# Performance work log

Hardware: AMD Instinct MI355X
Metric: run time of the kernel (lower is better)

Reference implementation:

```python
import jax, jax.numpy as jnp
import numpy as np

B, L, H, W = 4, 16, 4096, 128   # W == nfeat == nclass (required by out.reshape)
NHID = 256

def setup_inputs() -> dict:
    key = jax.random.key(0)
    k1, k2, k3, k4 = jax.random.split(key, 4)
    x = jax.random.normal(k1, (B, L, H, W), dtype=jnp.float32)
    # row-normalized-ish dense adjacency stand-in for the sparse normalized adj
    adj = jax.random.uniform(k2, (H, H), dtype=jnp.float32) / H
    # GraphConvolution params: support = input @ Wk; out = adj @ support + bk
    W1 = jax.random.normal(k3, (W, NHID), dtype=jnp.float32) / np.sqrt(W)
    b1 = jnp.zeros((NHID,), dtype=jnp.float32)
    W2 = jax.random.normal(k4, (NHID, W), dtype=jnp.float32) / np.sqrt(NHID)
    b2 = jnp.zeros((W,), dtype=jnp.float32)
    return {"x": x, "adj": adj, "W1": W1, "b1": b1, "W2": W2, "b2": b2}

def reference(x, adj, W1, b1, W2, b2):
    Bv, Lv, Hv, Wv = x.shape
    xf = x.reshape(Bv * Lv, Hv, Wv)                      # [BL, H, F]
    # gc1: transform then aggregate, fused over all slices (replaces per-slice loop)
    h = jnp.einsum('nm,bmf->bnf', adj, xf @ W1) + b1     # [BL, H, nhid]
    h = jax.nn.relu(h)
    # dropout: inference mode (training=False) -> identity
    out = jnp.einsum('nm,bmf->bnf', adj, h @ W2) + b2    # [BL, H, nclass]
    out = out.reshape(Bv, Lv, Hv, Wv)
    return jax.nn.log_softmax(out, axis=-1)
```

## Files before the change

kernel.cpp:

```cpp
#include <hip/hip_runtime.h>

typedef __attribute__((ext_vector_type(8))) __bf16 bf16x8;
typedef __attribute__((ext_vector_type(4))) float f32x4;
typedef __attribute__((ext_vector_type(16))) float f32x16;
typedef __attribute__((ext_vector_type(4))) int i32x4;
typedef __attribute__((ext_vector_type(8))) int i32x8;
typedef union { i32x8 v8; i32x4 v4[2]; } opnd;

__device__ __forceinline__ ushort f2b(float f) {
  union { float f; unsigned u; } v; v.f = f;
  unsigned u = v.u + 0x7fffu + ((v.u >> 16) & 1u);
  return (ushort)(u >> 16);
}

__device__ __forceinline__ unsigned fp4q(float v) {
  float a = __builtin_fabsf(v);
  unsigned q = (unsigned)(a > 0.25f) + (a > 0.75f) + (a > 1.25f) + (a > 1.75f)
             + (a > 2.5f) + (a > 3.5f) + (a > 5.0f);
  return q | (v < 0.0f ? 8u : 0u);
}
__device__ __forceinline__ ushort fp4pk4(float v0, float v1, float v2, float v3) {
  return (ushort)(fp4q(v0) | (fp4q(v1) << 4) | (fp4q(v2) << 8) | (fp4q(v3) << 12));
}

__device__ __forceinline__ long tiled_addr(long r, long k, int nkb) {
  return (((r >> 5) * nkb) + (k >> 6)) * 2048 + ((k & 16) ? 1024 : 0)
       + (((r & 31) + (((k >> 5) & 1) << 5)) << 4) + (k & 15);
}
__device__ __forceinline__ long tile4_addr(long r, long k, int nkb) {
  return (((r >> 5) * nkb) + (k >> 6)) * 1024
       + (((r & 31) + (((k >> 5) & 1) << 5)) << 4) + ((k & 31) >> 1);
}

__device__ __forceinline__ long remap_wg(int lin, int nwg, int gx) {
  long g = lin;
  if ((nwg & 7) == 0) {
    int cpx = nwg >> 3;
    int gyx = cpx / gx;
    int xcd = lin & 7, idx = lin >> 3;
    if ((gx & 3) == 0 && gyx >= 4 && (gyx & 3) == 0) {
      int st = idx >> 4, wi = idx & 15;
      int nstr = gx >> 2;
      int str = st % nstr, stc = st / nstr;
      int r = str * 4 + (wi & 3);
      int c2 = stc * 4 + (wi >> 2);
      g = (long)xcd * cpx + (long)c2 * gx + r;
    } else {
      g = (long)xcd * cpx + idx;
    }
  }
  return g;
}

__global__ __launch_bounds__(256) void cvtAdj4t(const float* __restrict__ in,
                                                unsigned char* __restrict__ out, long n) {
  long i = ((long)blockIdx.x * 256 + threadIdx.x) * 8;
  if (i >= n) return;
  float4 a = *(const float4*)(in + i);
  float4 b = *(const float4*)(in + i + 4);
  const float S = 24576.0f;
  ushort p0 = fp4pk4(a.x * S, a.y * S, a.z * S, a.w * S);
  ushort p1 = fp4pk4(b.x * S, b.y * S, b.z * S, b.w * S);
  long r = i >> 12;
  long k = i & 4095;
  *(int*)(out + tile4_addr(r, k, 64)) = (int)p0 | ((int)p1 << 16);
}

__global__ __launch_bounds__(256) void cvtX4t(const float* __restrict__ X,
                                              unsigned char* __restrict__ out4) {
  __shared__ float tile[32][33];
  const int tid = threadIdx.x;
  const long bl = blockIdx.z;
  const int m0 = blockIdx.y * 32;
  const int w0 = blockIdx.x * 32;
  const float* xb = X + (bl * 4096 + m0) * 128 + w0;
  int row = tid >> 3, cg = tid & 7;
  float4 v = *(const float4*)(xb + (long)row * 128 + cg * 4);
  tile[row][cg * 4 + 0] = v.x;
  tile[row][cg * 4 + 1] = v.y;
  tile[row][cg * 4 + 2] = v.z;
  tile[row][cg * 4 + 3] = v.w;
  __syncthreads();
  if (tid < 128) {
    int wv = tid & 31, mg = tid >> 5;
    unsigned word = 0;
#pragma unroll
    for (int i = 0; i < 8; ++i)
      word |= fp4q(tile[mg * 8 + i][wv]) << (4 * i);
    long r = bl * 128 + w0 + wv;
    long k = m0 + mg * 8;
    *(int*)(out4 + tile4_addr(r, k, 64)) = (int)word;
  }
}

__global__ __launch_bounds__(256) void prep_params(const float* __restrict__ W1,
                                                   const float* __restrict__ W2,
                                                   unsigned char* __restrict__ W1T8,
                                                   unsigned char* __restrict__ W2T8) {
  int idx = blockIdx.x * 256 + threadIdx.x;
  if (idx < 32768) {
    int f = idx >> 7, wv = idx & 127;
    float v = W1[wv * 256 + f] * 16.0f;
    int pk = __builtin_amdgcn_cvt_pk_fp8_f32(v, v, 0, 0);
    W1T8[tiled_addr(f, wv, 2)] = (unsigned char)(pk & 0xff);
  } else {
    int t = idx - 32768;
    int cc = t >> 8, f = t & 255;
    float v = W2[f * 128 + cc] * 16.0f;
    int pk = __builtin_amdgcn_cvt_pk_fp8_f32(v, v, 0, 0);
    W2T8[tiled_addr(cc, f, 4)] = (unsigned char)(pk & 0xff);
  }
}

__global__ __launch_bounds__(256, 3) void gemmS1(const unsigned char* __restrict__ A4,
                                                 const unsigned char* __restrict__ X4,
                                                 const unsigned char* __restrict__ W1T8,
                                                 const unsigned char* __restrict__ W2T8,
                                                 unsigned char* __restrict__ t2T4,
                                                 const float* __restrict__ b1,
                                                 int K, int gx) {
  __shared__ unsigned char S1buf[16384];
  __shared__ unsigned char hbuf[32768];
  const int tid = threadIdx.x;
  const int l = tid & 63;
  const int w = tid >> 6;
  long g = remap_wg(blockIdx.x, gridDim.x, gx);
  const long row0 = (g % gx) * 128;
  const long bl = g / gx;
  const int nkb = K >> 6;
  const int wr = w >> 1, wc = w & 1;
  const unsigned char* pA = A4 + (((row0 >> 5) + wr * 2) * (long)nkb) * 1024 + l * 16;
  const unsigned char* pB = X4 + ((bl * 4 + wc * 2) * (long)nkb) * 1024 + l * 16;

  f32x16 acc[2][2] = {};
  opnd aA[2], bA[2], aB[2], bB[2];
  const i32x4 z4 = {0, 0, 0, 0};
#pragma unroll
  for (int fi = 0; fi < 2; ++fi) {
    aA[fi].v4[1] = z4; aB[fi].v4[1] = z4;
    bA[fi].v4[1] = z4; bB[fi].v4[1] = z4;
  }

#define LOADG(KT, AV, BV) do { long off_ = (long)(KT) * 1024;                         \
    _Pragma("unroll") for (int fi = 0; fi < 2; ++fi)                                  \
      AV[fi].v4[0] = *(const i32x4*)(pA + (long)fi * nkb * 1024 + off_);              \
    _Pragma("unroll") for (int j = 0; j < 2; ++j)                                     \
      BV[j].v4[0] = *(const i32x4*)(pB + (long)j * nkb * 1024 + off_);                \
  } while (0)

#define MFMAS(AV, BV) do {                                                            \
    __builtin_amdgcn_s_setprio(1);                                                    \
    _Pragma("unroll") for (int fi = 0; fi < 2; ++fi)                                  \
      _Pragma("unroll") for (int j = 0; j < 2; ++j)                                   \
        acc[fi][j] = __builtin_amdgcn_mfma_scale_f32_32x32x64_f8f6f4(                 \
            AV[fi].v8, BV[j].v8, acc[fi][j], 4, 4, 0, 127, 0, 127);                   \
    __builtin_amdgcn_s_setprio(0); } while (0)

  const int nkt = K >> 6;
  LOADG(0, aA, bA);
  int kt = 0;
  for (; kt < nkt - 2; kt += 2) {
    LOADG(kt + 1, aB, bB);
    MFMAS(aA, bA);
    LOADG(kt + 2, aA, bA);
    MFMAS(aB, bB);
  }
  LOADG(nkt - 1, aB, bB);
  MFMAS(aA, bA);
  MFMAS(aB, bB);
#undef LOADG
#undef MFMAS

  const int hi = l >> 5;
#pragma unroll
  for (int fi = 0; fi < 2; ++fi) {
#pragma unroll
    for (int j = 0; j < 2; ++j) {
      int w_in = wc * 64 + j * 32 + (l & 31);
#pragma unroll
      for (int r = 0; r < 16; ++r) {
        int n = wr * 64 + fi * 32 + (r & 3) + 8 * (r >> 2) + 4 * hi;
        float v = acc[fi][j][r] * 0.125f;
        int pk = __builtin_amdgcn_cvt_pk_fp8_f32(v, v, 0, 0);
        S1buf[tiled_addr(n, w_in, 2)] = (unsigned char)(pk & 0xff);
      }
    }
  }
  __syncthreads();

#pragma unroll
  for (int hh = 0; hh < 2; ++hh) {
#pragma unroll
    for (int fi = 0; fi < 2; ++fi)
#pragma unroll
      for (int jb = 0; jb < 2; ++jb) acc[fi][jb] = (f32x16){};
#pragma unroll
    for (int kt1 = 0; kt1 < 2; ++kt1) {
#pragma unroll
      for (int jb = 0; jb < 2; ++jb) {
        opnd bw;
        const unsigned char* pW = W1T8 + (long)((hh * 4 + wc * 2 + jb) * 2 + kt1) * 2048 + l * 16;
        bw.v4[0] = *(const i32x4*)(pW);
        bw.v4[1] = *(const i32x4*)(pW + 1024);
#pragma unroll
        for (int fi = 0; fi < 2; ++fi) {
          opnd ah;
          const unsigned char* pS = S1buf + (long)((wr * 2 + fi) * 2 + kt1) * 2048 + l * 16;
          ah.v4[0] = *(const i32x4*)(pS);
          ah.v4[1] = *(const i32x4*)(pS + 1024);
          acc[fi][jb] = __builtin_amdgcn_mfma_scale_f32_32x32x64_f8f6f4(
              ah.v8, bw.v8, acc[fi][jb], 0, 0, 0, 127, 0, 127);
        }
      }
    }
#pragma unroll
    for (int fi = 0; fi < 2; ++fi) {
#pragma unroll
      for (int jb = 0; jb < 2; ++jb) {
        int f = hh * 128 + wc * 64 + jb * 32 + (l & 31);
        float bb = b1[f];
#pragma unroll
        for (int r = 0; r < 16; ++r) {
          int n = wr * 64 + fi * 32 + (r & 3) + 8 * (r >> 2) + 4 * hi;
          float v = fmaxf(acc[fi][jb][r] * (1.0f / 49152.0f) + bb, 0.0f) * 128.0f;
          int pk = __builtin_amdgcn_cvt_pk_fp8_f32(v, v, 0, 0);
          hbuf[tiled_addr(n, f, 4)] = (unsigned char)(pk & 0xff);
        }
      }
    }
  }
  __syncthreads();

#pragma unroll
  for (int fi = 0; fi < 2; ++fi)
#pragma unroll
    for (int jb = 0; jb < 2; ++jb) acc[fi][jb] = (f32x16){};
#pragma unroll
  for (int kt2 = 0; kt2 < 4; ++kt2) {
#pragma unroll
    for (int jb = 0; jb < 2; ++jb) {
      opnd bw;
      const unsigned char* pW = W2T8 + (long)((wc * 2 + jb) * 4 + kt2) * 2048 + l * 16;
      bw.v4[0] = *(const i32x4*)(pW);
      bw.v4[1] = *(const i32x4*)(pW + 1024);
#pragma unroll
      for (int fi = 0; fi < 2; ++fi) {
        opnd ah;
        const unsigned char* pH = hbuf + (long)((wr * 2 + fi) * 4 + kt2) * 2048 + l * 16;
        ah.v4[0] = *(const i32x4*)(pH);
        ah.v4[1] = *(const i32x4*)(pH + 1024);
        acc[fi][jb] = __builtin_amdgcn_mfma_scale_f32_32x32x64_f8f6f4(
            ah.v8, bw.v8, acc[fi][jb], 0, 0, 0, 127, 0, 127);
      }
    }
  }
  unsigned char* ob = t2T4 + bl * 262144;
#pragma unroll
  for (int fi = 0; fi < 2; ++fi) {
#pragma unroll
    for (int jb = 0; jb < 2; ++jb) {
      int cc = wc * 64 + jb * 32 + (l & 31);
#pragma unroll
      for (int run = 0; run < 4; ++run) {
        long n0 = row0 + wr * 64 + fi * 32 + 8 * run + 4 * hi;
        const float s = 0.125f;
        ushort pk = fp4pk4(acc[fi][jb][run * 4 + 0] * s, acc[fi][jb][run * 4 + 1] * s,
                           acc[fi][jb][run * 4 + 2] * s, acc[fi][jb][run * 4 + 3] * s);
        *(ushort*)(ob + tile4_addr(cc, n0, 64)) = pk;
      }
    }
  }
}

__global__ __launch_bounds__(512) void gemm256sm(const unsigned char* __restrict__ A4,
                                                 const unsigned char* __restrict__ B4,
                                                 float* __restrict__ out,
                                                 const float* __restrict__ bias,
                                                 float ooScale, int K, int gx,
                                                 int chunkBase) {
  __shared__ unsigned char ring[32768];
  const int tid = threadIdx.x;
  const int l = tid & 63;
  const int w = tid >> 6;
  int lin = blockIdx.x;
  const int nwg = gridDim.x;
  if ((nwg & 7) == 0) {
    int cpx = nwg >> 3;
    lin = (lin & 7) * cpx + (lin >> 3);
  }
  const long row0 = (long)(lin % gx) * 256;
  const long col0 = (long)(lin / gx) * 256;
  const int nkb = K >> 6;
  const unsigned char* sBp = B4 + (((col0 >> 5) + w) * (long)nkb) * 1024 + l * 16;
  unsigned char* ringw = ring + w * 1024;
  const unsigned char* ringr = ring + ((w & 1) * 4) * 1024 + l * 16;
  const unsigned char* pA = A4 + (((row0 + (w >> 1) * 64) >> 5) * (long)nkb) * 1024 + l * 16;

  f32x16 acc[2][4] = {};
  opnd bv[4], a0v[2], a1v[2], a2v[2];
  const i32x4 z4 = {0, 0, 0, 0};
#pragma unroll
  for (int j = 0; j < 4; ++j) bv[j].v4[1] = z4;
#pragma unroll
  for (int fi = 0; fi < 2; ++fi) { a0v[fi].v4[1] = z4; a1v[fi].v4[1] = z4; a2v[fi].v4[1] = z4; }

#define STGB(KT) __builtin_amdgcn_global_load_lds(                                    \
    (const unsigned int*)(const void*)(sBp + (long)(KT) * 1024),                      \
    (unsigned int*)(ringw + (((KT) & 3) << 13)), 16, 0, 0)
#define LOADA(KT, AV) do { long o_ = (long)(KT) * 1024;                               \
    AV[0].v4[0] = *(const i32x4*)(pA + o_);                                           \
    AV[1].v4[0] = *(const i32x4*)(pA + (long)nkb * 1024 + o_); } while (0)
#define LDB(KT) do { const unsigned char* p_ = ringr + (((KT) & 3) << 13);            \
    bv[0].v4[0] = *(const i32x4*)(p_);                                                \
    bv[1].v4[0] = *(const i32x4*)(p_ + 1024);                                         \
    bv[2].v4[0] = *(const i32x4*)(p_ + 2048);                                         \
    bv[3].v4[0] = *(const i32x4*)(p_ + 3072); } while (0)
#define MFMAS(AV) do { __builtin_amdgcn_s_setprio(1);                                 \
    _Pragma("unroll") for (int fi = 0; fi < 2; ++fi)                                  \
      _Pragma("unroll") for (int j = 0; j < 4; ++j)                                   \
        acc[fi][j] = __builtin_amdgcn_mfma_scale_f32_32x32x64_f8f6f4(                 \
            AV[fi].v8, bv[j].v8, acc[fi][j], 4, 4, 0, 127, 0, 127);                   \
    __builtin_amdgcn_s_setprio(0); } while (0)
#define BODY(KT, N, DOSTG, DOA, ALD, AUSE) do {                                       \
    LDB(KT);                                                                          \
    if (DOSTG) STGB((KT) + 3);                                                        \
    if (DOA) LOADA((KT) + 2, ALD);                                                    \
    asm volatile("s_waitcnt vmcnt(" N ")" ::: "memory");                              \
    MFMAS(AUSE);                                                                      \
    __builtin_amdgcn_s_barrier(); } while (0)

  const int nkt = K >> 6;
  STGB(0); STGB(1); STGB(2);
  LOADA(0, a0v); LOADA(1, a1v);
  asm volatile("s_waitcnt vmcnt(6)" ::: "memory");
  __builtin_amdgcn_s_barrier();

  BODY(0, "5", 1, 1, a2v, a0v);
  for (int kt = 1; kt + 6 <= nkt; kt += 3) {
    BODY(kt,     "6", 1, 1, a0v, a1v);
    BODY(kt + 1, "6", 1, 1, a1v, a2v);
    BODY(kt + 2, "6", 1, 1, a2v, a0v);
  }
  BODY(nkt - 3, "5", 0, 1, a0v, a1v);
  BODY(nkt - 2, "2", 0, 0, a0v, a2v);
  BODY(nkt - 1, "0", 0, 0, a0v, a0v);
#undef STGB
#undef LOADA
#undef LDB
#undef MFMAS
#undef BODY

  const int hi = l >> 5;
  const int bl = (int)(col0 >> 7) + (w & 1);
  float bb[4];
#pragma unroll
  for (int j = 0; j < 4; ++j) bb[j] = bias[j * 32 + (l & 31)];
#pragma unroll
  for (int fi = 0; fi < 2; ++fi) {
#pragma unroll
    for (int rr = 0; rr < 16; ++rr) {
      float v0 = acc[fi][0][rr] * ooScale + bb[0];
      float v1 = acc[fi][1][rr] * ooScale + bb[1];
      float v2 = acc[fi][2][rr] * ooScale + bb[2];
      float v3 = acc[fi][3][rr] * ooScale + bb[3];
      float m = fmaxf(fmaxf(v0, v1), fmaxf(v2, v3));
#pragma unroll
      for (int o = 16; o > 0; o >>= 1) m = fmaxf(m, __shfl_xor(m, o));
      float s = __expf(v0 - m) + __expf(v1 - m) + __expf(v2 - m) + __expf(v3 - m);
#pragma unroll
      for (int o = 16; o > 0; o >>= 1) s += __shfl_xor(s, o);
      float lse = m + __logf(s);
      long row = row0 + (w >> 1) * 64 + fi * 32 + ((rr & 3) + 8 * (rr >> 2) + 4 * hi);
      float* dst = out + ((long)(chunkBase + bl) * 4096 + row) * 128;
      dst[(l & 31)] = v0 - lse;
      dst[32 + (l & 31)] = v1 - lse;
      dst[64 + (l & 31)] = v2 - lse;
      dst[96 + (l & 31)] = v3 - lse;
    }
  }
}

extern "C" void kernel_launch(void* const* d_in, const int* in_sizes, int n_in,
                              void* d_out, int out_size, void* d_ws, size_t ws_size,
                              hipStream_t stream) {
  const float* x = (const float*)d_in[0];
  const float* adj = (const float*)d_in[1];
  const float* W1 = (const float*)d_in[2];
  const float* b1 = (const float*)d_in[3];
  const float* W2 = (const float*)d_in[4];
  const float* b2 = (const float*)d_in[5];
  float* out = (float*)d_out;
  char* ws = (char*)d_ws;

  unsigned char* adj4 = (unsigned char*)ws;
  unsigned char* W1T8 = (unsigned char*)(ws + 8388608);
  unsigned char* W2T8 = (unsigned char*)(ws + 8388608 + 32768);
  const size_t base = 9ull * 1024 * 1024;

  const int cands[6] = {64, 32, 16, 8, 4, 2};
  int c = 2;
  for (int t = 0; t < 6; ++t) {
    size_t need = base + (size_t)cands[t] * 524288;
    if (need <= ws_size) { c = cands[t]; break; }
  }
  unsigned char* x4T = (unsigned char*)(ws + base);
  unsigned char* t2T4 = x4T + (size_t)c * 262144;

  cvtAdj4t<<<8192, 256, 0, stream>>>(adj, adj4, (long)4096 * 4096);
  prep_params<<<256, 256, 0, stream>>>(W1, W2, W1T8, W2T8);

  int chunks = 64 / c;
  for (int cb = 0; cb < chunks; ++cb) {
    int base_bl = cb * c;
    const float* xc = x + (long)base_bl * 4096 * 128;

    cvtX4t<<<dim3(4, 128, c), 256, 0, stream>>>(xc, x4T);
    gemmS1<<<32 * c, 256, 0, stream>>>(adj4, x4T, W1T8, W2T8, t2T4, b1, 4096, 32);
    gemm256sm<<<16 * (c / 2), 512, 0, stream>>>(adj4, t2T4, out, b2,
                                                1.0f / 6291456.0f, 4096, 16, base_bl);
  }
}
```

Before: 246.9 us.

## Use hardware FP4 pack conversion and transposed MFMA to vectorize LDS epilogue stores

Replaces the comparison-ladder FP4 quantizer with the hardware scaled pk_fp4 conversion builtin where available, in the adjacency, X and output quantization paths. In gemmS1 it swaps the MFMA operand order so the accumulator comes out transposed. This lets the fp8 epilogues pack four values per word and write 32-bit LDS stores instead of single bytes. The 1/8 scale is folded into the MFMA exponent, and the bias is preloaded into shared memory already scaled. Rounding of the hardware FP4 conversion may differ from the hand-written thresholds, and the transposed layout has to match the tiled addressing exactly.

```diff
diff --git a/kernel.cpp b/kernel.cpp
--- a/kernel.cpp
+++ b/kernel.cpp
@@ -1,27 +1,23 @@
 #include <hip/hip_runtime.h>
 
-typedef __attribute__((ext_vector_type(8))) __bf16 bf16x8;
 typedef __attribute__((ext_vector_type(4))) float f32x4;
 typedef __attribute__((ext_vector_type(16))) float f32x16;
 typedef __attribute__((ext_vector_type(4))) int i32x4;
 typedef __attribute__((ext_vector_type(8))) int i32x8;
 typedef union { i32x8 v8; i32x4 v4[2]; } opnd;
 
-__device__ __forceinline__ ushort f2b(float f) {
-  union { float f; unsigned u; } v; v.f = f;
-  unsigned u = v.u + 0x7fffu + ((v.u >> 16) & 1u);
-  return (ushort)(u >> 16);
-}
-
 __device__ __forceinline__ unsigned fp4q(float v) {
   float a = __builtin_fabsf(v);
   unsigned q = (unsigned)(a > 0.25f) + (a > 0.75f) + (a > 1.25f) + (a > 1.75f)
              + (a > 2.5f) + (a > 3.5f) + (a > 5.0f);
   return q | (v < 0.0f ? 8u : 0u);
 }
-__device__ __forceinline__ ushort fp4pk4(float v0, float v1, float v2, float v3) {
-  return (ushort)(fp4q(v0) | (fp4q(v1) << 4) | (fp4q(v2) << 8) | (fp4q(v3) << 12));
-}
+
+#if __has_builtin(__builtin_amdgcn_cvt_scalef32_pk_fp4_f32)
+#define PKFP4(old, x, y, s) __builtin_amdgcn_cvt_scalef32_pk_fp4_f32((old), (x), (y), 1.0f, (s))
+#else
+#define PKFP4(old, x, y, s) ((old) | ((fp4q(x) | (fp4q(y) << 4)) << (8 * (s))))
+#endif
 
 __device__ __forceinline__ long tiled_addr(long r, long k, int nkb) {
   return (((r >> 5) * nkb) + (k >> 6)) * 2048 + ((k & 16) ? 1024 : 0)
@@ -59,11 +55,13 @@
   float4 a = *(const float4*)(in + i);
   float4 b = *(const float4*)(in + i + 4);
   const float S = 24576.0f;
-  ushort p0 = fp4pk4(a.x * S, a.y * S, a.z * S, a.w * S);
-  ushort p1 = fp4pk4(b.x * S, b.y * S, b.z * S, b.w * S);
+  unsigned word = PKFP4(0u, a.x * S, a.y * S, 0);
+  word = PKFP4(word, a.z * S, a.w * S, 1);
+  word = PKFP4(word, b.x * S, b.y * S, 2);
+  word = PKFP4(word, b.z * S, b.w * S, 3);
   long r = i >> 12;
   long k = i & 4095;
-  *(int*)(out + tile4_addr(r, k, 64)) = (int)p0 | ((int)p1 << 16);
+  *(int*)(out + tile4_addr(r, k, 64)) = (int)word;
 }
 
 __global__ __launch_bounds__(256) void cvtX4t(const float* __restrict__ X,
@@ -83,10 +81,13 @@
   __syncthreads();
   if (tid < 128) {
     int wv = tid & 31, mg = tid >> 5;
-    unsigned word = 0;
-#pragma unroll
-    for (int i = 0; i < 8; ++i)
-      word |= fp4q(tile[mg * 8 + i][wv]) << (4 * i);
+    float t[8];
+#pragma unroll
+    for (int i = 0; i < 8; ++i) t[i] = tile[mg * 8 + i][wv];
+    unsigned word = PKFP4(0u, t[0], t[1], 0);
+    word = PKFP4(word, t[2], t[3], 1);
+    word = PKFP4(word, t[4], t[5], 2);
+    word = PKFP4(word, t[6], t[7], 3);
     long r = bl * 128 + w0 + wv;
     long k = m0 + mg * 8;
     *(int*)(out4 + tile4_addr(r, k, 64)) = (int)word;
@@ -121,9 +122,11 @@
                                                  int K, int gx) {
   __shared__ unsigned char S1buf[16384];
   __shared__ unsigned char hbuf[32768];
+  __shared__ float b1s[256];
   const int tid = threadIdx.x;
   const int l = tid & 63;
   const int w = tid >> 6;
+  b1s[tid] = b1[tid] * 128.0f;
   long g = remap_wg(blockIdx.x, gridDim.x, gx);
   const long row0 = (g % gx) * 128;
   const long bl = g / gx;
@@ -153,7 +156,7 @@
     _Pragma("unroll") for (int fi = 0; fi < 2; ++fi)                                  \
       _Pragma("unroll") for (int j = 0; j < 2; ++j)                                   \
         acc[fi][j] = __builtin_amdgcn_mfma_scale_f32_32x32x64_f8f6f4(                 \
-            AV[fi].v8, BV[j].v8, acc[fi][j], 4, 4, 0, 127, 0, 127);                   \
+            BV[j].v8, AV[fi].v8, acc[fi][j], 4, 4, 0, 127, 0, 124);                   \
     __builtin_amdgcn_s_setprio(0); } while (0)
 
   const int nkt = K >> 6;
@@ -172,22 +175,27 @@
 #undef MFMAS
 
   const int hi = l >> 5;
+  const int ln = l & 31;
 #pragma unroll
   for (int fi = 0; fi < 2; ++fi) {
+    int n = (wr * 2 + fi) * 32 + ln;
 #pragma unroll
     for (int j = 0; j < 2; ++j) {
-      int w_in = wc * 64 + j * 32 + (l & 31);
-#pragma unroll
-      for (int r = 0; r < 16; ++r) {
-        int n = wr * 64 + fi * 32 + (r & 3) + 8 * (r >> 2) + 4 * hi;
-        float v = acc[fi][j][r] * 0.125f;
-        int pk = __builtin_amdgcn_cvt_pk_fp8_f32(v, v, 0, 0);
-        S1buf[tiled_addr(n, w_in, 2)] = (unsigned char)(pk & 0xff);
+      int wb = (wc * 2 + j) * 32 + 4 * hi;
+#pragma unroll
+      for (int r4 = 0; r4 < 4; ++r4) {
+        int w0 = wb + 8 * r4;
+        int word = __builtin_amdgcn_cvt_pk_fp8_f32(acc[fi][j][4 * r4 + 0],
+                                                   acc[fi][j][4 * r4 + 1], 0, false);
+        word = __builtin_amdgcn_cvt_pk_fp8_f32(acc[fi][j][4 * r4 + 2],
+                                               acc[fi][j][4 * r4 + 3], word, true);
+        *(int*)(S1buf + tiled_addr(n, w0, 2)) = word;
       }
     }
   }
   __syncthreads();
 
+  const float c1 = 128.0f / 49152.0f;
 #pragma unroll
   for (int hh = 0; hh < 2; ++hh) {
 #pragma unroll
@@ -198,33 +206,38 @@
     for (int kt1 = 0; kt1 < 2; ++kt1) {
 #pragma unroll
       for (int jb = 0; jb < 2; ++jb) {
-        opnd bw;
+        opnd aw;
         const unsigned char* pW = W1T8 + (long)((hh * 4 + wc * 2 + jb) * 2 + kt1) * 2048 + l * 16;
-        bw.v4[0] = *(const i32x4*)(pW);
-        bw.v4[1] = *(const i32x4*)(pW + 1024);
+        aw.v4[0] = *(const i32x4*)(pW);
+        aw.v4[1] = *(const i32x4*)(pW + 1024);
 #pragma unroll
         for (int fi = 0; fi < 2; ++fi) {
-          opnd ah;
+          opnd bs;
           const unsigned char* pS = S1buf + (long)((wr * 2 + fi) * 2 + kt1) * 2048 + l * 16;
-          ah.v4[0] = *(const i32x4*)(pS);
-          ah.v4[1] = *(const i32x4*)(pS + 1024);
+          bs.v4[0] = *(const i32x4*)(pS);
+          bs.v4[1] = *(const i32x4*)(pS + 1024);
           acc[fi][jb] = __builtin_amdgcn_mfma_scale_f32_32x32x64_f8f6f4(
-              ah.v8, bw.v8, acc[fi][jb], 0, 0, 0, 127, 0, 127);
+              aw.v8, bs.v8, acc[fi][jb], 0, 0, 0, 127, 0, 127);
         }
       }
     }
 #pragma unroll
-    for (int fi = 0; fi < 2; ++fi) {
-#pragma unroll
-      for (int jb = 0; jb < 2; ++jb) {
-        int f = hh * 128 + wc * 64 + jb * 32 + (l & 31);
-        float bb = b1[f];
-#pragma unroll
-        for (int r = 0; r < 16; ++r) {
-          int n = wr * 64 + fi * 32 + (r & 3) + 8 * (r >> 2) + 4 * hi;
-          float v = fmaxf(acc[fi][jb][r] * (1.0f / 49152.0f) + bb, 0.0f) * 128.0f;
-          int pk = __builtin_amdgcn_cvt_pk_fp8_f32(v, v, 0, 0);
-          hbuf[tiled_addr(n, f, 4)] = (unsigned char)(pk & 0xff);
+    for (int jb = 0; jb < 2; ++jb) {
+      int fb = (hh * 4 + wc * 2 + jb) * 32 + 4 * hi;
+#pragma unroll
+      for (int r4 = 0; r4 < 4; ++r4) {
+        int f0 = fb + 8 * r4;
+        float4 bb = *(const float4*)(b1s + f0);
+#pragma unroll
+        for (int fi = 0; fi < 2; ++fi) {
+          int n = (wr * 2 + fi) * 32 + ln;
+          float v0 = fmaxf(fmaf(acc[fi][jb][4 * r4 + 0], c1, bb.x), 0.0f);
+          float v1 = fmaxf(fmaf(acc[fi][jb][4 * r4 + 1], c1, bb.y), 0.0f);
+          float v2 = fmaxf(fmaf(acc[fi][jb][4 * r4 + 2], c1, bb.z), 0.0f);
+          float v3 = fmaxf(fmaf(acc[fi][jb][4 * r4 + 3], c1, bb.w), 0.0f);
+          int word = __builtin_amdgcn_cvt_pk_fp8_f32(v0, v1, 0, false);
+          word = __builtin_amdgcn_cvt_pk_fp8_f32(v2, v3, word, true);
+          *(int*)(hbuf + tiled_addr(n, f0, 4)) = word;
         }
       }
     }
@@ -259,14 +272,16 @@
   for (int fi = 0; fi < 2; ++fi) {
 #pragma unroll
     for (int jb = 0; jb < 2; ++jb) {
-      int cc = wc * 64 + jb * 32 + (l & 31);
+      int cc = wc * 64 + jb * 32 + ln;
 #pragma unroll
       for (int run = 0; run < 4; ++run) {
         long n0 = row0 + wr * 64 + fi * 32 + 8 * run + 4 * hi;
         const float s = 0.125f;
-        ushort pk = fp4pk4(acc[fi][jb][run * 4 + 0] * s, acc[fi][jb][run * 4 + 1] * s,
-                           acc[fi][jb][run * 4 + 2] * s, acc[fi][jb][run * 4 + 3] * s);
-        *(ushort*)(ob + tile4_addr(cc, n0, 64)) = pk;
+        unsigned pkw = PKFP4(0u, acc[fi][jb][run * 4 + 0] * s,
+                                 acc[fi][jb][run * 4 + 1] * s, 0);
+        pkw = PKFP4(pkw, acc[fi][jb][run * 4 + 2] * s,
+                         acc[fi][jb][run * 4 + 3] * s, 1);
+        *(ushort*)(ob + tile4_addr(cc, n0, 64)) = (ushort)pkw;
       }
     }
   }
```

Result: faster. 235.0 us (-4.8%).
